# Optimization experiments

Measured on AMD Instinct MI355X. Metric: run time of the kernel, lower is better.

## Reference

```python
import jax, jax.numpy as jnp
import numpy as np

N, T, F, HID, HEADS, E = 10000, 6, 64, 64, 4, 160000


def gat_conv(x, W, a_src, a_dst, bias, src, dst, n, concat):
    """PyG-style GATConv (self-loops already appended to src/dst).
    x: [n, in]; W: [in, H*C]; a_src/a_dst: [H, C]; returns ([n, H*C] or [n, C], alpha [E', H])."""
    H, C = a_src.shape
    xw = (x @ W).reshape(n, H, C)
    # per-edge unnormalized attention logits
    al = (xw * a_src).sum(-1)[src] + (xw * a_dst).sum(-1)[dst]  # [E', H]
    al = jax.nn.leaky_relu(al, 0.2)
    # segment softmax over destination neighborhoods
    m = jax.ops.segment_max(al, dst, num_segments=n)
    ex = jnp.exp(al - m[dst])
    s = jax.ops.segment_sum(ex, dst, num_segments=n)
    alpha = ex / (s[dst] + 1e-16)
    out = jax.ops.segment_sum(xw[src] * alpha[:, :, None], dst, num_segments=n)  # [n, H, C]
    out = out.reshape(n, H * C) if concat else out.mean(axis=1)
    return out + bias, alpha


def setup_inputs() -> dict:
    key = jax.random.key(0)
    ks = jax.random.split(key, 12)
    sc = 0.05
    return {
        "x": jax.random.normal(ks[0], (N, T, F), jnp.float32),
        "edge_index": jax.random.randint(ks[1], (2, E), 0, N, jnp.int64),
        "W0": jax.random.normal(ks[2], (F, HID), jnp.float32) * sc,
        "a_src0": jax.random.normal(ks[3], (HEADS, HID // HEADS), jnp.float32) * sc,
        "a_dst0": jax.random.normal(ks[4], (HEADS, HID // HEADS), jnp.float32) * sc,
        "b0": jnp.zeros((HID,), jnp.float32),
        "W1": jax.random.normal(ks[5], (HID, HEADS * HID), jnp.float32) * sc,
        "a_src1": jax.random.normal(ks[6], (HEADS, HID), jnp.float32) * sc,
        "a_dst1": jax.random.normal(ks[7], (HEADS, HID), jnp.float32) * sc,
        "b1": jnp.zeros((HID,), jnp.float32),
        "ln_g": jnp.ones((HID,), jnp.float32),
        "ln_b": jnp.zeros((HID,), jnp.float32),
        "W_ih": jax.random.normal(ks[8], (3 * HID, HID), jnp.float32) * sc,
        "W_hh": jax.random.normal(ks[9], (3 * HID, HID), jnp.float32) * sc,
        "b_ih": jnp.zeros((3 * HID,), jnp.float32),
        "b_hh": jnp.zeros((3 * HID,), jnp.float32),
    }


def reference(x, edge_index, W0, a_src0, a_dst0, b0, W1, a_src1, a_dst1, b1,
              ln_g, ln_b, W_ih, W_hh, b_ih, b_hh):
    n = x.shape[0]
    loops = jnp.arange(n)
    src = jnp.concatenate([edge_index[0], loops])  # add self loops
    dst = jnp.concatenate([edge_index[1], loops])

    def gat_step(_, xt):
        h, _a = gat_conv(xt, W0, a_src0, a_dst0, b0, src, dst, n, True)
        h = jax.nn.elu(h)  # dropout is identity in eval mode
        h, alpha = gat_conv(h, W1, a_src1, a_dst1, b1, src, dst, n, False)
        h = jax.nn.elu(h)
        mu = h.mean(-1, keepdims=True)
        v = ((h - mu) ** 2).mean(-1, keepdims=True)
        h = (h - mu) / jnp.sqrt(v + 1e-5) * ln_g + ln_b
        return None, (h, alpha)

    _, (Hs, alphas) = jax.lax.scan(gat_step, None, jnp.moveaxis(x, 1, 0))  # Hs: [T, n, HID]

    def gru_step(h, xt):
        gi = xt @ W_ih.T + b_ih
        gh = h @ W_hh.T + b_hh
        ir, iz, ig = jnp.split(gi, 3, axis=-1)
        hr, hz, hg = jnp.split(gh, 3, axis=-1)
        r = jax.nn.sigmoid(ir + hr)
        z = jax.nn.sigmoid(iz + hz)
        g = jnp.tanh(ig + r * hg)
        return (1.0 - z) * g + z * h, None

    h0 = jnp.zeros((n, W_hh.shape[1]), x.dtype)
    hT, _ = jax.lax.scan(gru_step, h0, Hs)  # last GRU output == last hidden (1 layer)
    attn_edge_index = jnp.stack([src, dst])
    return hT, alphas[-1], attn_edge_index
```

## Files before the change

kernel.cpp:

```cpp
#include <hip/hip_runtime.h>
#include <hip/hip_bf16.h>
#include <cstdint>
#include <cstddef>

#define N_NODES 10000
#define T_STEPS 6
#define F_IN    64
#define HID     64
#define HEADS   4
#define E_EDGES 160000
#define EP      (E_EDGES + N_NODES)
#define TN      (T_STEPS * N_NODES)
#define NTILES  (TN / 16)
#define CAP     96

typedef __hip_bfloat16 bf16;
typedef __attribute__((ext_vector_type(8))) short short8;
typedef __attribute__((ext_vector_type(4))) float floatx4;

__device__ __forceinline__ float bfu(unsigned short s) { return __uint_as_float((unsigned)s << 16); }
__device__ __forceinline__ unsigned short f2bu(float f) {
    bf16 b = __float2bfloat16(f);
    return *(unsigned short*)&b;
}
__device__ __forceinline__ void lds_fence() {
    asm volatile("s_waitcnt lgkmcnt(0)" ::: "memory");
}
__device__ __forceinline__ int xcd_swizzle(int b, int nblk) {
    int q = nblk >> 3, r = nblk & 7;
    int x = b & 7, j = b >> 3;
    return (x < r ? x * (q + 1) : r * (q + 1) + (x - r) * q) + j;
}


__global__ void k_scatter(const int* ei, int* fill,
                          int* csr_src, int* csr_eid, float* out_ei) {
    int e = blockIdx.x * blockDim.x + threadIdx.x;
    if (e >= EP) return;
    int src = (e < E_EDGES) ? ei[e] : (e - E_EDGES);
    int dst = (e < E_EDGES) ? ei[E_EDGES + e] : (e - E_EDGES);
    int pos = atomicAdd(&fill[dst], 1);
    if (pos < CAP) {
        csr_src[dst * CAP + pos] = src;
        csr_eid[dst * CAP + pos] = e;
    }
    out_ei[e] = (float)src;
    out_ei[EP + e] = (float)dst;
}


__global__ __launch_bounds__(256) void k_prep(const float* __restrict__ W0,
                                              const float* __restrict__ W1,
                                              const float* __restrict__ a_src0,
                                              const float* __restrict__ a_dst0,
                                              const float* __restrict__ a_src1,
                                              const float* __restrict__ a_dst1,
                                              const float* __restrict__ W_ih,
                                              const float* __restrict__ W_hh,
                                              bf16* __restrict__ W0bt,
                                              bf16* __restrict__ W1bt,
                                              bf16* __restrict__ wihb,
                                              bf16* __restrict__ whhb,
                                              float* __restrict__ P0s,
                                              float* __restrict__ P0d,
                                              float* __restrict__ P1s,
                                              float* __restrict__ P1d) {
    int b = blockIdx.x, tid = threadIdx.x;
    if (b == 176) {
        int h = tid >> 6, k = tid & 63;
        float ps = 0.f, pd = 0.f;
        for (int c = 0; c < 64; c++) {
            float wv = W1[k * 256 + h * 64 + c];
            ps += wv * a_src1[h * 64 + c];
            pd += wv * a_dst1[h * 64 + c];
        }
        P1s[h * 64 + k] = ps;
        P1d[h * 64 + k] = pd;
        return;
    }
    if (b == 177) {
        int h = tid >> 6, k = tid & 63;
        float ps = 0.f, pd = 0.f;
        for (int c = 0; c < 16; c++) {
            float wv = W0[k * 64 + h * 16 + c];
            ps += wv * a_src0[h * 16 + c];
            pd += wv * a_dst0[h * 16 + c];
        }
        P0s[h * 64 + k] = ps;
        P0d[h * 64 + k] = pd;
        return;
    }
    int i = b * 256 + tid;
    if (i < 4096) {
        W0bt[i] = __float2bfloat16(W0[(i & 63) * 64 + (i >> 6)]);
    } else if (i < 20480) {
        int j = i - 4096; int c = j >> 8, K = j & 255;
        W1bt[j] = __float2bfloat16(W1[(K & 63) * 256 + (K >> 6) * 64 + c]);
    } else if (i < 32768) {
        wihb[i - 20480] = __float2bfloat16(W_ih[i - 20480]);
    } else {
        whhb[i - 32768] = __float2bfloat16(W_hh[i - 32768]);
    }
}

__global__ __launch_bounds__(256) void k_gemm0(const float* __restrict__ x,
                                               const bf16* __restrict__ W0bt,
                                               const float* __restrict__ P0s,
                                               const float* __restrict__ P0d,
                                               bf16* __restrict__ XW0b,
                                               float* __restrict__ ALS0,
                                               float* __restrict__ ALD0) {
    __shared__ __align__(16) bf16 wt[64 * 64];
    int tid = threadIdx.x;
    for (int i = tid; i < 512; i += 256)
        ((short8*)wt)[i] = ((const short8*)W0bt)[i];
    __syncthreads();
    int wv = tid >> 6, lane = tid & 63;
    int tile = blockIdx.x * 4 + wv;
    if (tile >= NTILES) return;
    int rb = tile * 16;
    int m = lane & 15, quad = lane >> 4;
    int row = rb + m;
    int t = row / N_NODES, n = row - t * N_NODES;
    const float* xr = x + ((size_t)n * T_STEPS + t) * F_IN + quad * 8;
    short8 a0, a1;
#pragma unroll
    for (int j = 0; j < 8; j++) {
        a0[j] = (short)f2bu(xr[j]);
        a1[j] = (short)f2bu(xr[32 + j]);
    }
    floatx4 acc[4];
#pragma unroll
    for (int ct = 0; ct < 4; ct++) {
        short8 bb0 = *(const short8*)(wt + (ct * 16 + m) * 64 + quad * 8);
        short8 bb1 = *(const short8*)(wt + (ct * 16 + m) * 64 + 32 + quad * 8);
        floatx4 a = {0.f, 0.f, 0.f, 0.f};
        a = __builtin_amdgcn_mfma_f32_16x16x32_bf16(a0, bb0, a, 0, 0, 0);
        a = __builtin_amdgcn_mfma_f32_16x16x32_bf16(a1, bb1, a, 0, 0, 0);
        acc[ct] = a;
    }
    short8 p0, p1;
#pragma unroll
    for (int j = 0; j < 8; j++) {
        int k0 = quad * 8 + j, k1 = 32 + quad * 8 + j;
        float v0 = 0.f, v1 = 0.f;
        if (m < 4)      { v0 = P0s[m * 64 + k0];       v1 = P0s[m * 64 + k1]; }
        else if (m < 8) { v0 = P0d[(m - 4) * 64 + k0]; v1 = P0d[(m - 4) * 64 + k1]; }
        p0[j] = (short)f2bu(v0);
        p1[j] = (short)f2bu(v1);
    }
    floatx4 ac5 = {0.f, 0.f, 0.f, 0.f};
    ac5 = __builtin_amdgcn_mfma_f32_16x16x32_bf16(a0, p0, ac5, 0, 0, 0);
    ac5 = __builtin_amdgcn_mfma_f32_16x16x32_bf16(a1, p1, ac5, 0, 0, 0);
#pragma unroll
    for (int ct = 0; ct < 4; ct++)
#pragma unroll
        for (int r = 0; r < 4; r++)
            XW0b[(size_t)(rb + quad * 4 + r) * 64 + ct * 16 + m] = __float2bfloat16(acc[ct][r]);
#pragma unroll
    for (int r = 0; r < 4; r++) {
        int orow = rb + quad * 4 + r;
        if (m < 4)      ALS0[orow * 4 + m] = ac5[r];
        else if (m < 8) ALD0[orow * 4 + (m - 4)] = ac5[r];
    }
}

__global__ __launch_bounds__(256) void k_fused0(const int* __restrict__ fill,
                                                const int* __restrict__ csr_src,
                                                const bf16* __restrict__ XW0b,
                                                const float* __restrict__ ALS0,
                                                const float* __restrict__ ALD0,
                                                const float* __restrict__ b0,
                                                const float* __restrict__ P1s,
                                                const float* __restrict__ P1d,
                                                bf16* __restrict__ H0b,
                                                float* __restrict__ ALS1,
                                                float* __restrict__ ALD1) {
    __shared__ int srcs[CAP][16];
    int tid = threadIdx.x;
    int wv = tid >> 6, lane = tid & 63;
    int sub = lane >> 4, il = lane & 15;
    int g = wv * 4 + sub;
    int tile = xcd_swizzle(blockIdx.x, NTILES);
    int wid = tile * 16 + g;
    int t = wid / N_NODES, n = wid - t * N_NODES;
    int deg = min(fill[n], CAP);
    int rs = n * CAP;
    int tb = t * N_NODES;
    int hsel = il >> 2;
    float adh = ALD0[(size_t)wid * 4 + hsel];
    for (int idx = il; idx < deg; idx += 16)
        srcs[idx][g] = csr_src[rs + idx];
    lds_fence();
    float ssum = 0.f, a0 = 0.f, a1 = 0.f, a2 = 0.f, a3 = 0.f;
    const bf16* hrow = XW0b + (size_t)tb * 64 + il * 4;
    const float* alsb = ALS0 + (size_t)tb * 4 + hsel;
    for (int k = 0; k < deg; k++) {
        int sx = srcs[k][g];
        float l = alsb[(size_t)sx * 4] + adh;
        l = l > 0.f ? l : 0.2f * l;
        float e = __expf(fminf(l, 80.f));
        ssum += e;
        ushort4 u = *(const ushort4*)(hrow + (size_t)sx * 64);
        a0 += e * bfu(u.x); a1 += e * bfu(u.y);
        a2 += e * bfu(u.z); a3 += e * bfu(u.w);
    }
    float iv = 1.f / (ssum + 1e-16f);
    float4 bv = *(const float4*)(b0 + il * 4);
    float v0 = a0 * iv + bv.x; v0 = v0 > 0.f ? v0 : (__expf(v0) - 1.f);
    float v1 = a1 * iv + bv.y; v1 = v1 > 0.f ? v1 : (__expf(v1) - 1.f);
    float v2 = a2 * iv + bv.z; v2 = v2 > 0.f ? v2 : (__expf(v2) - 1.f);
    float v3 = a3 * iv + bv.w; v3 = v3 > 0.f ? v3 : (__expf(v3) - 1.f);
    ushort4 o4;
    o4.x = f2bu(v0); o4.y = f2bu(v1); o4.z = f2bu(v2); o4.w = f2bu(v3);
    *(ushort4*)(H0b + (size_t)wid * 64 + il * 4) = o4;

    float ps[4], pd[4];
#pragma unroll
    for (int h = 0; h < 4; h++) {
        float4 s4 = *(const float4*)(P1s + h * 64 + il * 4);
        float4 d4 = *(const float4*)(P1d + h * 64 + il * 4);
        ps[h] = v0 * s4.x + v1 * s4.y + v2 * s4.z + v3 * s4.w;
        pd[h] = v0 * d4.x + v1 * d4.y + v2 * d4.z + v3 * d4.w;
    }
#pragma unroll
    for (int o = 1; o <= 8; o <<= 1) {
#pragma unroll
        for (int h = 0; h < 4; h++) {
            ps[h] += __shfl_xor(ps[h], o, 64);
            pd[h] += __shfl_xor(pd[h], o, 64);
        }
    }
    if (il == 0) {
        float4 w1; w1.x = ps[0]; w1.y = ps[1]; w1.z = ps[2]; w1.w = ps[3];
        *(float4*)(ALS1 + (size_t)wid * 4) = w1;
        float4 w2; w2.x = pd[0]; w2.y = pd[1]; w2.z = pd[2]; w2.w = pd[3];
        *(float4*)(ALD1 + (size_t)wid * 4) = w2;
    }
}

__global__ __launch_bounds__(256) void k_fused1(const int* __restrict__ fill,
                                                const int* __restrict__ csr_src,
                                                const int* __restrict__ csr_eid,
                                                const bf16* __restrict__ H0b,
                                                const float* __restrict__ ALS1,
                                                const float* __restrict__ ALD1,
                                                const bf16* __restrict__ W1bt,
                                                const float* __restrict__ b1,
                                                const float* __restrict__ ln_g,
                                                const float* __restrict__ ln_b,
                                                bf16* __restrict__ HSb,
                                                float* __restrict__ out_alpha) {
    __shared__ __align__(16) union SM {
        int srcs[CAP][16];
        struct { bf16 ast[16][264]; float ost[16][68]; } q;
    } sm;
    int tid = threadIdx.x;
    int wv = tid >> 6, lane = tid & 63;
    int sub = lane >> 4, il = lane & 15;
    int g = wv * 4 + sub;
    int tile = xcd_swizzle(blockIdx.x, NTILES);
    int wid = tile * 16 + g;
    int t = wid / N_NODES, n = wid - t * N_NODES;
    int deg = min(fill[n], CAP);
    int rs = n * CAP;
    int tb = t * N_NODES;
    bool do_out = (t == T_STEPS - 1);
    float4 ad4 = *(const float4*)(ALD1 + (size_t)wid * 4);
    for (int idx = il; idx < deg; idx += 16)
        sm.srcs[idx][g] = csr_src[rs + idx];
    lds_fence();
    float s0 = 0.f, s1 = 0.f, s2 = 0.f, s3 = 0.f;
    float acc[4][4];
#pragma unroll
    for (int h = 0; h < 4; h++)
#pragma unroll
        for (int j = 0; j < 4; j++) acc[h][j] = 0.f;
    const bf16* hrow = H0b + (size_t)tb * 64 + il * 4;
    const float* alsb = ALS1 + (size_t)tb * 4;
    for (int k = 0; k < deg; k++) {
        int sx = sm.srcs[k][g];
        float4 as = *(const float4*)(alsb + (size_t)sx * 4);
        float l0 = as.x + ad4.x; l0 = l0 > 0.f ? l0 : 0.2f * l0;
        float l1 = as.y + ad4.y; l1 = l1 > 0.f ? l1 : 0.2f * l1;
        float l2 = as.z + ad4.z; l2 = l2 > 0.f ? l2 : 0.2f * l2;
        float l3 = as.w + ad4.w; l3 = l3 > 0.f ? l3 : 0.2f * l3;
        float e0 = __expf(fminf(l0, 80.f));
        float e1 = __expf(fminf(l1, 80.f));
        float e2 = __expf(fminf(l2, 80.f));
        float e3 = __expf(fminf(l3, 80.f));
        s0 += e0; s1 += e1; s2 += e2; s3 += e3;
        ushort4 u = *(const ushort4*)(hrow + (size_t)sx * 64);
        float x0 = bfu(u.x), x1 = bfu(u.y), x2 = bfu(u.z), x3 = bfu(u.w);
        acc[0][0] += e0 * x0; acc[0][1] += e0 * x1; acc[0][2] += e0 * x2; acc[0][3] += e0 * x3;
        acc[1][0] += e1 * x0; acc[1][1] += e1 * x1; acc[1][2] += e1 * x2; acc[1][3] += e1 * x3;
        acc[2][0] += e2 * x0; acc[2][1] += e2 * x1; acc[2][2] += e2 * x2; acc[2][3] += e2 * x3;
        acc[3][0] += e3 * x0; acc[3][1] += e3 * x1; acc[3][2] += e3 * x2; acc[3][3] += e3 * x3;
    }
    float iv0 = 1.f / (s0 + 1e-16f), iv1 = 1.f / (s1 + 1e-16f);
    float iv2 = 1.f / (s2 + 1e-16f), iv3 = 1.f / (s3 + 1e-16f);

    if (do_out) {
        for (int idx = il; idx < deg; idx += 16) {
            int sx = sm.srcs[idx][g];
            float4 as = *(const float4*)(alsb + (size_t)sx * 4);
            float l0 = as.x + ad4.x; l0 = l0 > 0.f ? l0 : 0.2f * l0;
            float l1 = as.y + ad4.y; l1 = l1 > 0.f ? l1 : 0.2f * l1;
            float l2 = as.z + ad4.z; l2 = l2 > 0.f ? l2 : 0.2f * l2;
            float l3 = as.w + ad4.w; l3 = l3 > 0.f ? l3 : 0.2f * l3;
            float4 o4;
            o4.x = __expf(fminf(l0, 80.f)) * iv0;
            o4.y = __expf(fminf(l1, 80.f)) * iv1;
            o4.z = __expf(fminf(l2, 80.f)) * iv2;
            o4.w = __expf(fminf(l3, 80.f)) * iv3;
            int eid = csr_eid[rs + idx];
            *(float4*)(out_alpha + (size_t)eid * 4) = o4;
        }
    }

    __syncthreads();
    float ivh[4] = { iv0, iv1, iv2, iv3 };
#pragma unroll
    for (int h = 0; h < 4; h++) {
        ushort4 o4;
        o4.x = f2bu(acc[h][0] * ivh[h]);
        o4.y = f2bu(acc[h][1] * ivh[h]);
        o4.z = f2bu(acc[h][2] * ivh[h]);
        o4.w = f2bu(acc[h][3] * ivh[h]);
        *(ushort4*)&sm.q.ast[g][h * 64 + il * 4] = o4;
    }
    __syncthreads();
    int m = il, quad = sub;
    floatx4 ga = {0.f, 0.f, 0.f, 0.f};
    const bf16* wrow = W1bt + (size_t)(wv * 16 + m) * 256 + quad * 8;
#pragma unroll
    for (int kb = 0; kb < 8; kb++) {
        short8 afk = *(const short8*)&sm.q.ast[m][kb * 32 + quad * 8];
        short8 bfk = *(const short8*)(wrow + kb * 32);
        ga = __builtin_amdgcn_mfma_f32_16x16x32_bf16(afk, bfk, ga, 0, 0, 0);
    }
#pragma unroll
    for (int r = 0; r < 4; r++)
        sm.q.ost[quad * 4 + r][wv * 16 + m] = ga[r];
    __syncthreads();
    int row = wv * 4 + quad;
    float4 vv = *(const float4*)&sm.q.ost[row][m * 4];
    float4 bb = *(const float4*)(b1 + m * 4);
    float v0 = vv.x * 0.25f + bb.x; v0 = v0 > 0.f ? v0 : (__expf(v0) - 1.f);
    float v1 = vv.y * 0.25f + bb.y; v1 = v1 > 0.f ? v1 : (__expf(v1) - 1.f);
    float v2 = vv.z * 0.25f + bb.z; v2 = v2 > 0.f ? v2 : (__expf(v2) - 1.f);
    float v3 = vv.w * 0.25f + bb.w; v3 = v3 > 0.f ? v3 : (__expf(v3) - 1.f);
    float sv = v0 + v1 + v2 + v3;
#pragma unroll
    for (int o = 1; o <= 8; o <<= 1) sv += __shfl_xor(sv, o, 64);
    float mu = sv * (1.f / 64.f);
    float d0 = v0 - mu, d1 = v1 - mu, d2 = v2 - mu, d3 = v3 - mu;
    float qv = d0 * d0 + d1 * d1 + d2 * d2 + d3 * d3;
#pragma unroll
    for (int o = 1; o <= 8; o <<= 1) qv += __shfl_xor(qv, o, 64);
    float rinv = rsqrtf(qv * (1.f / 64.f) + 1e-5f);
    float4 gg = *(const float4*)(ln_g + m * 4);
    float4 lb = *(const float4*)(ln_b + m * 4);
    ushort4 ho;
    ho.x = f2bu(d0 * rinv * gg.x + lb.x);
    ho.y = f2bu(d1 * rinv * gg.y + lb.y);
    ho.z = f2bu(d2 * rinv * gg.z + lb.z);
    ho.w = f2bu(d3 * rinv * gg.w + lb.w);
    *(ushort4*)(HSb + (size_t)(tile * 16 + row) * 64 + m * 4) = ho;
}

__global__ __launch_bounds__(256) void k_gru(const bf16* __restrict__ HSb,
                                             const bf16* __restrict__ wihb,
                                             const float* __restrict__ b_ih,
                                             const bf16* __restrict__ whhb,
                                             const float* __restrict__ b_hh,
                                             float* __restrict__ outh) {
    __shared__ __align__(16) bf16 hbuf[16 * 72];
    int tid = threadIdx.x;
    int wv = tid >> 6, lane = tid & 63;
    int rb = blockIdx.x * 16;
    int m = lane & 15, quad = lane >> 4;
    int fb = wv * 16;
    const int rowR = (fb + m) * 64, rowZ = (64 + fb + m) * 64, rowG = (128 + fb + m) * 64;
    short8 Br0 = *(const short8*)(wihb + rowR + quad * 8);
    short8 Br1 = *(const short8*)(wihb + rowR + 32 + quad * 8);
    short8 Bz0 = *(const short8*)(wihb + rowZ + quad * 8);
    short8 Bz1 = *(const short8*)(wihb + rowZ + 32 + quad * 8);
    short8 Bg0 = *(const short8*)(wihb + rowG + quad * 8);
    short8 Bg1 = *(const short8*)(wihb + rowG + 32 + quad * 8);
    short8 Cr0 = *(const short8*)(whhb + rowR + quad * 8);
    short8 Cr1 = *(const short8*)(whhb + rowR + 32 + quad * 8);
    short8 Cz0 = *(const short8*)(whhb + rowZ + quad * 8);
    short8 Cz1 = *(const short8*)(whhb + rowZ + 32 + quad * 8);
    short8 Cg0 = *(const short8*)(whhb + rowG + quad * 8);
    short8 Cg1 = *(const short8*)(whhb + rowG + 32 + quad * 8);
    float biR = b_ih[fb + m], biZ = b_ih[64 + fb + m], biG = b_ih[128 + fb + m];
    float bhR = b_hh[fb + m], bhZ = b_hh[64 + fb + m], bhG = b_hh[128 + fb + m];
    float hprev[4] = {0.f, 0.f, 0.f, 0.f};

    for (int t = 0; t < T_STEPS; t++) {
        const bf16* xr = HSb + ((size_t)t * N_NODES + rb + m) * 64;
        short8 ax0 = *(const short8*)(xr + quad * 8);
        short8 ax1 = *(const short8*)(xr + 32 + quad * 8);
        short8 ah0, ah1;
        if (t > 0) {
            ah0 = *(const short8*)(hbuf + m * 72 + quad * 8);
            ah1 = *(const short8*)(hbuf + m * 72 + 32 + quad * 8);
        }
        __syncthreads();
        floatx4 aR = {0.f, 0.f, 0.f, 0.f}, aZ = {0.f, 0.f, 0.f, 0.f};
        floatx4 aGi = {0.f, 0.f, 0.f, 0.f}, aGh = {0.f, 0.f, 0.f, 0.f};
        aR = __builtin_amdgcn_mfma_f32_16x16x32_bf16(ax0, Br0, aR, 0, 0, 0);
        aR = __builtin_amdgcn_mfma_f32_16x16x32_bf16(ax1, Br1, aR, 0, 0, 0);
        aZ = __builtin_amdgcn_mfma_f32_16x16x32_bf16(ax0, Bz0, aZ, 0, 0, 0);
        aZ = __builtin_amdgcn_mfma_f32_16x16x32_bf16(ax1, Bz1, aZ, 0, 0, 0);
        aGi = __builtin_amdgcn_mfma_f32_16x16x32_bf16(ax0, Bg0, aGi, 0, 0, 0);
        aGi = __builtin_amdgcn_mfma_f32_16x16x32_bf16(ax1, Bg1, aGi, 0, 0, 0);
        if (t > 0) {
            aR = __builtin_amdgcn_mfma_f32_16x16x32_bf16(ah0, Cr0, aR, 0, 0, 0);
            aR = __builtin_amdgcn_mfma_f32_16x16x32_bf16(ah1, Cr1, aR, 0, 0, 0);
            aZ = __builtin_amdgcn_mfma_f32_16x16x32_bf16(ah0, Cz0, aZ, 0, 0, 0);
            aZ = __builtin_amdgcn_mfma_f32_16x16x32_bf16(ah1, Cz1, aZ, 0, 0, 0);
            aGh = __builtin_amdgcn_mfma_f32_16x16x32_bf16(ah0, Cg0, aGh, 0, 0, 0);
            aGh = __builtin_amdgcn_mfma_f32_16x16x32_bf16(ah1, Cg1, aGh, 0, 0, 0);
        }
#pragma unroll
        for (int r = 0; r < 4; r++) {
            float rr = 1.f / (1.f + __expf(-(aR[r] + biR + bhR)));
            float z  = 1.f / (1.f + __expf(-(aZ[r] + biZ + bhZ)));
            float g  = tanhf(aGi[r] + biG + rr * (aGh[r] + bhG));
            hprev[r] = (1.f - z) * g + z * hprev[r];
        }
        if (t < T_STEPS - 1) {
#pragma unroll
            for (int r = 0; r < 4; r++)
                hbuf[(quad * 4 + r) * 72 + fb + m] = __float2bfloat16(hprev[r]);
            __syncthreads();
        }
    }
#pragma unroll
    for (int r = 0; r < 4; r++)
        outh[(size_t)(rb + quad * 4 + r) * 64 + fb + m] = hprev[r];
}


extern "C" void kernel_launch(void* const* d_in, const int* in_sizes, int n_in,
                              void* d_out, int out_size, void* d_ws, size_t ws_size,
                              hipStream_t stream) {
    const float* x      = (const float*)d_in[0];
    const int*   ei     = (const int*)d_in[1];
    const float* W0     = (const float*)d_in[2];
    const float* a_src0 = (const float*)d_in[3];
    const float* a_dst0 = (const float*)d_in[4];
    const float* b0     = (const float*)d_in[5];
    const float* W1     = (const float*)d_in[6];
    const float* a_src1 = (const float*)d_in[7];
    const float* a_dst1 = (const float*)d_in[8];
    const float* b1     = (const float*)d_in[9];
    const float* ln_g   = (const float*)d_in[10];
    const float* ln_b   = (const float*)d_in[11];
    const float* W_ih   = (const float*)d_in[12];
    const float* W_hh   = (const float*)d_in[13];
    const float* b_ih   = (const float*)d_in[14];
    const float* b_hh   = (const float*)d_in[15];
    float* out = (float*)d_out;

    char* w = (char*)d_ws;
    size_t off = 0;
    auto take = [&](size_t bytes) -> void* {
        void* p = w + off;
        off = (off + bytes + 255) & ~(size_t)255;
        return p;
    };
    int*   fill    = (int*)take(N_NODES * 4);
    int*   csr_src = (int*)take((size_t)N_NODES * CAP * 4);
    int*   csr_eid = (int*)take((size_t)N_NODES * CAP * 4);
    bf16*  XW0b    = (bf16*)take((size_t)TN * 64 * 2);
    float* ALS0    = (float*)take((size_t)TN * 4 * 4);
    float* ALD0    = (float*)take((size_t)TN * 4 * 4);
    bf16*  H0b     = (bf16*)take((size_t)TN * 64 * 2);
    float* P0s     = (float*)take(256 * 4);
    float* P0d     = (float*)take(256 * 4);
    float* P1s     = (float*)take(256 * 4);
    float* P1d     = (float*)take(256 * 4);
    float* ALS1    = (float*)take((size_t)TN * 4 * 4);
    float* ALD1    = (float*)take((size_t)TN * 4 * 4);
    bf16*  HSb     = (bf16*)take((size_t)TN * 64 * 2);
    bf16*  W0bt    = (bf16*)take(4096 * 2);
    bf16*  W1bt    = (bf16*)take(16384 * 2);
    bf16*  wihb    = (bf16*)take(12288 * 2);
    bf16*  whhb    = (bf16*)take(12288 * 2);
    (void)ws_size; (void)in_sizes; (void)n_in; (void)out_size;

    const int B = 256;
    float* out_ei = out + (size_t)N_NODES * HID + (size_t)EP * HEADS;

    hipMemsetAsync(fill, 0, N_NODES * 4, stream);
    k_prep<<<178, B, 0, stream>>>(W0, W1, a_src0, a_dst0, a_src1, a_dst1, W_ih, W_hh,
                                  W0bt, W1bt, wihb, whhb, P0s, P0d, P1s, P1d);
    k_scatter<<<(EP + B - 1) / B, B, 0, stream>>>(ei, fill, csr_src, csr_eid, out_ei);

    const int GT = (NTILES + 3) / 4;
    k_gemm0<<<GT, B, 0, stream>>>(x, W0bt, P0s, P0d, XW0b, ALS0, ALD0);
    k_fused0<<<NTILES, B, 0, stream>>>(fill, csr_src, XW0b, ALS0, ALD0, b0,
                                       P1s, P1d, H0b, ALS1, ALD1);

    k_fused1<<<NTILES, B, 0, stream>>>(fill, csr_src, csr_eid, H0b, ALS1, ALD1,
                                       W1bt, b1, ln_g, ln_b, HSb,
                                       out + (size_t)N_NODES * HID);

    k_gru<<<N_NODES / 16, B, 0, stream>>>(HSb, wihb, b_ih, whhb, b_hh, out);
}
```

Before: 212.4 us.

## Precompute per-edge attention exps in parallel into LDS before aggregation loop

Splits the second GAT layer's neighbor loop into two phases for nodes with degree up to 64. First, the 16 lanes of each group compute the leaky-relu/exp attention weights for different edges in parallel and store them and the source ids in LDS, with a shuffle reduction for the softmax denominator. Second, the serial aggregation loop reads these weights instead of redoing the gather of the logits and four exps per edge per lane. The alpha output reuses the stored exps rather than recomputing them. Nodes with higher degree fall back to the old serial path, which adds a divergent branch and more LDS use (16-bit source ids).

```diff
diff --git a/kernel.cpp b/kernel.cpp
--- a/kernel.cpp
+++ b/kernel.cpp
@@ -252,7 +252,7 @@
                                                 bf16* __restrict__ HSb,
                                                 float* __restrict__ out_alpha) {
     __shared__ __align__(16) union SM {
-        int srcs[CAP][16];
+        struct { float exv[4][4][64][4]; unsigned short srcs[4][4][64]; } p;
         struct { bf16 ast[16][264]; float ost[16][68]; } q;
     } sm;
     int tid = threadIdx.x;
@@ -267,54 +267,109 @@
     int tb = t * N_NODES;
     bool do_out = (t == T_STEPS - 1);
     float4 ad4 = *(const float4*)(ALD1 + (size_t)wid * 4);
-    for (int idx = il; idx < deg; idx += 16)
-        sm.srcs[idx][g] = csr_src[rs + idx];
-    lds_fence();
-    float s0 = 0.f, s1 = 0.f, s2 = 0.f, s3 = 0.f;
     float acc[4][4];
 #pragma unroll
     for (int h = 0; h < 4; h++)
 #pragma unroll
         for (int j = 0; j < 4; j++) acc[h][j] = 0.f;
+    float iv0, iv1, iv2, iv3;
     const bf16* hrow = H0b + (size_t)tb * 64 + il * 4;
     const float* alsb = ALS1 + (size_t)tb * 4;
-    for (int k = 0; k < deg; k++) {
-        int sx = sm.srcs[k][g];
-        float4 as = *(const float4*)(alsb + (size_t)sx * 4);
-        float l0 = as.x + ad4.x; l0 = l0 > 0.f ? l0 : 0.2f * l0;
-        float l1 = as.y + ad4.y; l1 = l1 > 0.f ? l1 : 0.2f * l1;
-        float l2 = as.z + ad4.z; l2 = l2 > 0.f ? l2 : 0.2f * l2;
-        float l3 = as.w + ad4.w; l3 = l3 > 0.f ? l3 : 0.2f * l3;
-        float e0 = __expf(fminf(l0, 80.f));
-        float e1 = __expf(fminf(l1, 80.f));
-        float e2 = __expf(fminf(l2, 80.f));
-        float e3 = __expf(fminf(l3, 80.f));
-        s0 += e0; s1 += e1; s2 += e2; s3 += e3;
-        ushort4 u = *(const ushort4*)(hrow + (size_t)sx * 64);
-        float x0 = bfu(u.x), x1 = bfu(u.y), x2 = bfu(u.z), x3 = bfu(u.w);
-        acc[0][0] += e0 * x0; acc[0][1] += e0 * x1; acc[0][2] += e0 * x2; acc[0][3] += e0 * x3;
-        acc[1][0] += e1 * x0; acc[1][1] += e1 * x1; acc[1][2] += e1 * x2; acc[1][3] += e1 * x3;
-        acc[2][0] += e2 * x0; acc[2][1] += e2 * x1; acc[2][2] += e2 * x2; acc[2][3] += e2 * x3;
-        acc[3][0] += e3 * x0; acc[3][1] += e3 * x1; acc[3][2] += e3 * x2; acc[3][3] += e3 * x3;
-    }
-    float iv0 = 1.f / (s0 + 1e-16f), iv1 = 1.f / (s1 + 1e-16f);
-    float iv2 = 1.f / (s2 + 1e-16f), iv3 = 1.f / (s3 + 1e-16f);
-
-    if (do_out) {
-        for (int idx = il; idx < deg; idx += 16) {
-            int sx = sm.srcs[idx][g];
+
+    int mdf = (deg <= 64) ? deg : 0;
+    mdf = max(mdf, __shfl_xor(mdf, 16, 64));
+    mdf = max(mdf, __shfl_xor(mdf, 32, 64));
+    int nbf = (mdf + 15) >> 4;
+
+    if (deg <= 64) {
+        float s0 = 0.f, s1 = 0.f, s2 = 0.f, s3 = 0.f;
+        for (int b = 0; b < nbf; b++) {
+            int idxe = b * 16 + il;
+            bool valid = idxe < deg;
+            int src = csr_src[valid ? rs + idxe : rs];
+            float4 as = *(const float4*)(alsb + (size_t)src * 4);
+            float l0 = as.x + ad4.x; l0 = l0 > 0.f ? l0 : 0.2f * l0;
+            float l1 = as.y + ad4.y; l1 = l1 > 0.f ? l1 : 0.2f * l1;
+            float l2 = as.z + ad4.z; l2 = l2 > 0.f ? l2 : 0.2f * l2;
+            float l3 = as.w + ad4.w; l3 = l3 > 0.f ? l3 : 0.2f * l3;
+            float e0 = valid ? __expf(fminf(l0, 80.f)) : 0.f;
+            float e1 = valid ? __expf(fminf(l1, 80.f)) : 0.f;
+            float e2 = valid ? __expf(fminf(l2, 80.f)) : 0.f;
+            float e3 = valid ? __expf(fminf(l3, 80.f)) : 0.f;
+            s0 += e0; s1 += e1; s2 += e2; s3 += e3;
+            float4 ex4; ex4.x = e0; ex4.y = e1; ex4.z = e2; ex4.w = e3;
+            if (valid) {
+                *(float4*)&sm.p.exv[wv][sub][idxe][0] = ex4;
+                sm.p.srcs[wv][sub][idxe] = (unsigned short)src;
+            }
+        }
+#pragma unroll
+        for (int o = 1; o <= 8; o <<= 1) {
+            s0 += __shfl_xor(s0, o, 64); s1 += __shfl_xor(s1, o, 64);
+            s2 += __shfl_xor(s2, o, 64); s3 += __shfl_xor(s3, o, 64);
+        }
+        iv0 = 1.f / (s0 + 1e-16f); iv1 = 1.f / (s1 + 1e-16f);
+        iv2 = 1.f / (s2 + 1e-16f); iv3 = 1.f / (s3 + 1e-16f);
+        lds_fence();
+        if (do_out) {
+            for (int idxe = il; idxe < deg; idxe += 16) {
+                float4 ex4 = *(const float4*)&sm.p.exv[wv][sub][idxe][0];
+                float4 o4;
+                o4.x = ex4.x * iv0; o4.y = ex4.y * iv1;
+                o4.z = ex4.z * iv2; o4.w = ex4.w * iv3;
+                int eid = csr_eid[rs + idxe];
+                *(float4*)(out_alpha + (size_t)eid * 4) = o4;
+            }
+        }
+        for (int k = 0; k < deg; k++) {
+            float4 ex = *(const float4*)&sm.p.exv[wv][sub][k][0];
+            int sx = sm.p.srcs[wv][sub][k];
+            ushort4 u = *(const ushort4*)(hrow + (size_t)sx * 64);
+            float x0 = bfu(u.x), x1 = bfu(u.y), x2 = bfu(u.z), x3 = bfu(u.w);
+            acc[0][0] += ex.x * x0; acc[0][1] += ex.x * x1; acc[0][2] += ex.x * x2; acc[0][3] += ex.x * x3;
+            acc[1][0] += ex.y * x0; acc[1][1] += ex.y * x1; acc[1][2] += ex.y * x2; acc[1][3] += ex.y * x3;
+            acc[2][0] += ex.z * x0; acc[2][1] += ex.z * x1; acc[2][2] += ex.z * x2; acc[2][3] += ex.z * x3;
+            acc[3][0] += ex.w * x0; acc[3][1] += ex.w * x1; acc[3][2] += ex.w * x2; acc[3][3] += ex.w * x3;
+        }
+    } else {
+        float s0 = 0.f, s1 = 0.f, s2 = 0.f, s3 = 0.f;
+        for (int k = 0; k < deg; k++) {
+            int sx = csr_src[rs + k];
             float4 as = *(const float4*)(alsb + (size_t)sx * 4);
             float l0 = as.x + ad4.x; l0 = l0 > 0.f ? l0 : 0.2f * l0;
             float l1 = as.y + ad4.y; l1 = l1 > 0.f ? l1 : 0.2f * l1;
             float l2 = as.z + ad4.z; l2 = l2 > 0.f ? l2 : 0.2f * l2;
             float l3 = as.w + ad4.w; l3 = l3 > 0.f ? l3 : 0.2f * l3;
-            float4 o4;
-            o4.x = __expf(fminf(l0, 80.f)) * iv0;
-            o4.y = __expf(fminf(l1, 80.f)) * iv1;
-            o4.z = __expf(fminf(l2, 80.f)) * iv2;
-            o4.w = __expf(fminf(l3, 80.f)) * iv3;
-            int eid = csr_eid[rs + idx];
-            *(float4*)(out_alpha + (size_t)eid * 4) = o4;
+            float e0 = __expf(fminf(l0, 80.f));
+            float e1 = __expf(fminf(l1, 80.f));
+            float e2 = __expf(fminf(l2, 80.f));
+            float e3 = __expf(fminf(l3, 80.f));
+            s0 += e0; s1 += e1; s2 += e2; s3 += e3;
+            ushort4 u = *(const ushort4*)(hrow + (size_t)sx * 64);
+            float x0 = bfu(u.x), x1 = bfu(u.y), x2 = bfu(u.z), x3 = bfu(u.w);
+            acc[0][0] += e0 * x0; acc[0][1] += e0 * x1; acc[0][2] += e0 * x2; acc[0][3] += e0 * x3;
+            acc[1][0] += e1 * x0; acc[1][1] += e1 * x1; acc[1][2] += e1 * x2; acc[1][3] += e1 * x3;
+            acc[2][0] += e2 * x0; acc[2][1] += e2 * x1; acc[2][2] += e2 * x2; acc[2][3] += e2 * x3;
+            acc[3][0] += e3 * x0; acc[3][1] += e3 * x1; acc[3][2] += e3 * x2; acc[3][3] += e3 * x3;
+        }
+        iv0 = 1.f / (s0 + 1e-16f); iv1 = 1.f / (s1 + 1e-16f);
+        iv2 = 1.f / (s2 + 1e-16f); iv3 = 1.f / (s3 + 1e-16f);
+        if (do_out) {
+            for (int idxe = il; idxe < deg; idxe += 16) {
+                int sx = csr_src[rs + idxe];
+                float4 as = *(const float4*)(alsb + (size_t)sx * 4);
+                float l0 = as.x + ad4.x; l0 = l0 > 0.f ? l0 : 0.2f * l0;
+                float l1 = as.y + ad4.y; l1 = l1 > 0.f ? l1 : 0.2f * l1;
+                float l2 = as.z + ad4.z; l2 = l2 > 0.f ? l2 : 0.2f * l2;
+                float l3 = as.w + ad4.w; l3 = l3 > 0.f ? l3 : 0.2f * l3;
+                float4 o4;
+                o4.x = __expf(fminf(l0, 80.f)) * iv0;
+                o4.y = __expf(fminf(l1, 80.f)) * iv1;
+                o4.z = __expf(fminf(l2, 80.f)) * iv2;
+                o4.w = __expf(fminf(l3, 80.f)) * iv3;
+                int eid = csr_eid[rs + idxe];
+                *(float4*)(out_alpha + (size_t)eid * 4) = o4;
+            }
         }
     }
 
```

After: 201.4 us. 1.05x faster.
